# Optimization experiments

Hardware: AMD Instinct MI355X
Metric: run time of the kernel (lower is better)

## Reference

```python
import jax, jax.numpy as jnp
import numpy as np

N = 100000
E = 640000
IN_CH = 64
HID = 128
HEADS = [4, 4, 1]
BN_EPS = 1e-5
NEG_SLOPE = 0.2  # GATConv default leaky relu slope


def setup_inputs() -> dict:
    key = jax.random.key(0)
    ks = iter(jax.random.split(key, 48))
    nrm = lambda shape, s=0.1: jax.random.normal(next(ks), shape, jnp.float32) * s
    return dict(
        x=jax.random.normal(next(ks), (N, IN_CH), jnp.float32),
        edge_index=jax.random.randint(next(ks), (2, E), 0, N),
        edge_weight=jax.random.uniform(next(ks), (E,), jnp.float32),
        Wproj=nrm((IN_CH, HID)), bproj=jnp.zeros((HID,), jnp.float32),
        gat_W=nrm((3, HID, HID)), att_src=nrm((3, HID)), att_dst=nrm((3, HID)),
        att_edge=nrm((3, HID)), lin_edge_W=nrm((3, HID)),
        gat_bias=jnp.zeros((3, HID), jnp.float32),
        bn_gamma=jnp.ones((3, HID), jnp.float32), bn_beta=jnp.zeros((3, HID), jnp.float32),
        bn_mean=nrm((3, HID), 0.05),
        bn_var=jax.random.uniform(next(ks), (3, HID), jnp.float32, 0.5, 1.5),
        ew_W1=nrm((3, 32)), ew_b1=jnp.zeros((3, 32), jnp.float32),
        ew_W2=nrm((3, 32)), ew_b2=jnp.zeros((3,), jnp.float32),
        symptom_attention=jnp.ones((HID,), jnp.float32),
        clf_W1=nrm((HID, 64)), clf_b1=jnp.zeros((64,), jnp.float32),
        clf_bn_gamma=jnp.ones((64,), jnp.float32), clf_bn_beta=jnp.zeros((64,), jnp.float32),
        clf_bn_mean=nrm((64,), 0.05),
        clf_bn_var=jax.random.uniform(next(ks), (64,), jnp.float32, 0.5, 1.5),
        clf_W2=nrm((64, 32)), clf_b2=jnp.zeros((32,), jnp.float32),
        clf_W3=nrm((32, 2)), clf_b3=jnp.zeros((2,), jnp.float32),
    )


def _bn(x, g, b, m, v):
    # eval-mode BatchNorm with running stats
    return (x - m) * jax.lax.rsqrt(v + BN_EPS) * g + b


def reference(x, edge_index, edge_weight, Wproj, bproj, gat_W, att_src, att_dst,
              att_edge, lin_edge_W, gat_bias, bn_gamma, bn_beta, bn_mean, bn_var,
              ew_W1, ew_b1, ew_W2, ew_b2, symptom_attention, clf_W1, clf_b1,
              clf_bn_gamma, clf_bn_beta, clf_bn_mean, clf_bn_var, clf_W2, clf_b2,
              clf_W3, clf_b3):
    n = x.shape[0]
    loop = jnp.arange(n)
    src = jnp.concatenate([edge_index[0], loop])  # [E+N] self loops appended
    dst = jnp.concatenate([edge_index[1], loop])
    h = x @ Wproj + bproj  # input projection -> [N, HID]
    for i, H in enumerate(HEADS):
        C = HID // H
        # edge attention MLP: Linear(1,32)->ReLU->Linear(32,1)->Sigmoid on raw edge_weight
        eh = jax.nn.relu(edge_weight[:, None] * ew_W1[i][None, :] + ew_b1[i])
        ea = jax.nn.sigmoid(eh @ ew_W2[i] + ew_b2[i])  # [E]
        few = edge_weight * ea  # final edge weight [E]
        # self-loop edge attr fill_value='mean'
        e_attr = jnp.concatenate([few, jnp.broadcast_to(jnp.mean(few), (n,))])  # [E+N]
        # GATConv
        xl = (h @ gat_W[i]).reshape(n, H, C)
        a_src = jnp.sum(xl * att_src[i].reshape(H, C), axis=-1)  # [N,H]
        a_dst = jnp.sum(xl * att_dst[i].reshape(H, C), axis=-1)  # [N,H]
        e_lin = (e_attr[:, None] * lin_edge_W[i][None, :]).reshape(-1, H, C)
        a_edge = jnp.sum(e_lin * att_edge[i].reshape(H, C), axis=-1)  # [E+N,H]
        alpha = jax.nn.leaky_relu(a_src[src] + a_dst[dst] + a_edge, NEG_SLOPE)
        amax = jax.ops.segment_max(alpha, dst, num_segments=n)
        ex = jnp.exp(alpha - amax[dst])
        denom = jax.ops.segment_sum(ex, dst, num_segments=n)
        w = ex / (denom[dst] + 1e-16)  # segment softmax over incoming edges
        out = jax.ops.segment_sum(w[:, :, None] * xl[src], dst, num_segments=n)
        h = out.reshape(n, HID) + gat_bias[i]
        h = jax.nn.elu(_bn(h, bn_gamma[i], bn_beta[i], bn_mean[i], bn_var[i]))
        # dropout is identity in eval mode
    h = h * symptom_attention
    c = jax.nn.relu(h @ clf_W1 + clf_b1)
    c = _bn(c, clf_bn_gamma, clf_bn_beta, clf_bn_mean, clf_bn_var)
    c = jax.nn.relu(c @ clf_W2 + clf_b2)
    logits = c @ clf_W3 + clf_b3
    return logits
```

## Files before the change

### kernel.cpp

```cpp
#include <hip/hip_runtime.h>
#include <hip/hip_fp16.h>
#include <math.h>

#define NN 100000
#define EE 640000
#define ENL (EE + NN)
#define HIDD 128

constexpr float BN_EPS = 1e-5f;

template<int KDIM, int NC, int EPI, int H>
__global__ __launch_bounds__(256) void k_gemm(
    const float* __restrict__ A, const float* __restrict__ W,
    const float* __restrict__ bias, float* __restrict__ out, int nrows,
    const float* __restrict__ att_s, const float* __restrict__ att_d,
    float* __restrict__ a_src, float* __restrict__ a_dst,
    const float* __restrict__ bng, const float* __restrict__ bnb,
    const float* __restrict__ bnm, const float* __restrict__ bnv)
{
    constexpr int TXN = NC / 4;
    constexpr int TYN = 256 / TXN;
    constexpr int RPT = 64 / TYN;
    __shared__ float Al[64][36];
    __shared__ float Wl[32][NC];
    const int t = threadIdx.x;
    const int tx = t % TXN, ty = t / TXN;
    const long rowBase = (long)blockIdx.x * 64;
    float acc[RPT][4];
#pragma unroll
    for (int r = 0; r < RPT; ++r) { acc[r][0]=0.f; acc[r][1]=0.f; acc[r][2]=0.f; acc[r][3]=0.f; }

    for (int kk = 0; kk < KDIM; kk += 32) {
#pragma unroll
        for (int j = 0; j < 2; ++j) {
            int idx = t + j * 256;
            int r = idx >> 3;
            int k4 = (idx & 7) << 2;
            long gr = rowBase + r;
            float4 v = make_float4(0.f, 0.f, 0.f, 0.f);
            if (gr < nrows) v = *(const float4*)(A + gr * KDIM + kk + k4);
            *(float4*)&Al[r][k4] = v;
        }
        constexpr int WLOAD = (32 * NC / 4) / 256;
#pragma unroll
        for (int j = 0; j < WLOAD; ++j) {
            int idx = t + j * 256;
            int k = idx / TXN;
            int c4 = (idx % TXN) << 2;
            *(float4*)&Wl[k][c4] = *(const float4*)(W + (long)(kk + k) * NC + c4);
        }
        __syncthreads();
#pragma unroll
        for (int k = 0; k < 32; ++k) {
            float4 wv = *(float4*)&Wl[k][tx * 4];
#pragma unroll
            for (int r = 0; r < RPT; ++r) {
                float av = Al[ty * RPT + r][k];
                acc[r][0] = fmaf(av, wv.x, acc[r][0]);
                acc[r][1] = fmaf(av, wv.y, acc[r][1]);
                acc[r][2] = fmaf(av, wv.z, acc[r][2]);
                acc[r][3] = fmaf(av, wv.w, acc[r][3]);
            }
        }
        __syncthreads();
    }

    const int col0 = tx * 4;
    if constexpr (EPI == 0) {
        float4 b4 = *(const float4*)(bias + col0);
#pragma unroll
        for (int r = 0; r < RPT; ++r) {
            long row = rowBase + ty * RPT + r;
            if (row < nrows) {
                float4 o = make_float4(acc[r][0] + b4.x, acc[r][1] + b4.y,
                                       acc[r][2] + b4.z, acc[r][3] + b4.w);
                *(float4*)(out + row * NC + col0) = o;
            }
        }
    } else if constexpr (EPI == 1) {
        __half* outh = reinterpret_cast<__half*>(out);
        float as4[4], ad4[4];
#pragma unroll
        for (int c = 0; c < 4; ++c) { as4[c] = att_s[col0 + c]; ad4[c] = att_d[col0 + c]; }
        constexpr int G = TXN / H;
#pragma unroll
        for (int r = 0; r < RPT; ++r) {
            long row = rowBase + ty * RPT + r;
            if (row < nrows) {
                union { __half2 h2[2]; uint2 u; } pk;
                pk.h2[0] = __floats2half2_rn(acc[r][0], acc[r][1]);
                pk.h2[1] = __floats2half2_rn(acc[r][2], acc[r][3]);
                *(uint2*)(outh + row * NC + col0) = pk.u;
            }
            float ps = 0.f, pd = 0.f;
#pragma unroll
            for (int c = 0; c < 4; ++c) {
                ps = fmaf(acc[r][c], as4[c], ps);
                pd = fmaf(acc[r][c], ad4[c], pd);
            }
#pragma unroll
            for (int m_ = 1; m_ < G; m_ <<= 1) {
                ps += __shfl_xor(ps, m_, 64);
                pd += __shfl_xor(pd, m_, 64);
            }
            if ((tx & (G - 1)) == 0 && row < nrows) {
                int h = tx / G;
                a_src[row * H + h] = ps;
                a_dst[row * H + h] = pd;
            }
        }
    } else {
        float4 b4 = *(const float4*)(bias + col0);
        float4 g4 = *(const float4*)(bng + col0);
        float4 be4 = *(const float4*)(bnb + col0);
        float4 m4 = *(const float4*)(bnm + col0);
        float4 v4 = *(const float4*)(bnv + col0);
        float s0 = rsqrtf(v4.x + BN_EPS) * g4.x;
        float s1 = rsqrtf(v4.y + BN_EPS) * g4.y;
        float s2 = rsqrtf(v4.z + BN_EPS) * g4.z;
        float s3 = rsqrtf(v4.w + BN_EPS) * g4.w;
#pragma unroll
        for (int r = 0; r < RPT; ++r) {
            long row = rowBase + ty * RPT + r;
            if (row < nrows) {
                float o0 = fmaxf(acc[r][0] + b4.x, 0.f);
                float o1 = fmaxf(acc[r][1] + b4.y, 0.f);
                float o2 = fmaxf(acc[r][2] + b4.z, 0.f);
                float o3 = fmaxf(acc[r][3] + b4.w, 0.f);
                float4 o = make_float4((o0 - m4.x) * s0 + be4.x,
                                       (o1 - m4.y) * s1 + be4.y,
                                       (o2 - m4.z) * s2 + be4.z,
                                       (o3 - m4.w) * s3 + be4.w);
                *(float4*)(out + row * NC + col0) = o;
            }
        }
    }
}

__global__ void k_prep(const float* __restrict__ lew, const float* __restrict__ ae,
                       float* __restrict__ scal, int H)
{
    __shared__ float p[128];
    int t = threadIdx.x;
    p[t] = lew[t] * ae[t];
    __syncthreads();
    if (t == 0) scal[0] = 0.f;
    if (t < H) {
        int Cc = 128 / H;
        float s = 0.f;
        for (int c = 0; c < Cc; ++c) s += p[t * Cc + c];
        scal[4 + t] = s;
    }
}

__global__ __launch_bounds__(256) void k_edgemlp(
    const float* __restrict__ ew, const float* __restrict__ W1,
    const float* __restrict__ b1, const float* __restrict__ W2,
    const float* __restrict__ b2, float* __restrict__ few,
    float* __restrict__ sumfew)
{
    __shared__ float red[4];
    int e = blockIdx.x * 256 + threadIdx.x;
    float f = 0.f;
    if (e < EE) {
        float w = ew[e];
        float acc = b2[0];
#pragma unroll
        for (int j = 0; j < 32; ++j) {
            float t_ = fmaf(w, W1[j], b1[j]);
            t_ = fmaxf(t_, 0.f);
            acc = fmaf(t_, W2[j], acc);
        }
        f = w / (1.f + __expf(-acc));
        few[e] = f;
    }
    float s = f;
#pragma unroll
    for (int m_ = 1; m_ < 64; m_ <<= 1) s += __shfl_xor(s, m_, 64);
    int lane = threadIdx.x & 63, wid = threadIdx.x >> 6;
    if (lane == 0) red[wid] = s;
    __syncthreads();
    if (threadIdx.x == 0) atomicAdd(sumfew, red[0] + red[1] + red[2] + red[3]);
}

__global__ __launch_bounds__(256) void k_hist(const int* __restrict__ edst, int* __restrict__ cnt)
{
    int e = blockIdx.x * 256 + threadIdx.x;
    if (e < ENL) {
        int d = (e < EE) ? edst[e] : (e - EE);
        atomicAdd(&cnt[d], 1);
    }
}

__global__ __launch_bounds__(256) void k_scan1(const int* __restrict__ cnt,
                                               int* __restrict__ tmp, int* __restrict__ part)
{
    __shared__ int s1[256];
    int t = threadIdx.x;
    int i = blockIdx.x * 256 + t;
    int x = (i < NN) ? cnt[i] : 0;
    s1[t] = x;
    __syncthreads();
#pragma unroll
    for (int off = 1; off < 256; off <<= 1) {
        int v_ = (t >= off) ? s1[t - off] : 0;
        __syncthreads();
        s1[t] += v_;
        __syncthreads();
    }
    if (i < NN) tmp[i] = s1[t] - x;
    if (t == 255) part[blockIdx.x] = s1[255];
}

__global__ void k_scan2(int* __restrict__ part, int nb)
{
    __shared__ int s1[512];
    int t = threadIdx.x;
    int x = (t < nb) ? part[t] : 0;
    s1[t] = x;
    __syncthreads();
#pragma unroll
    for (int off = 1; off < 512; off <<= 1) {
        int v_ = (t >= off) ? s1[t - off] : 0;
        __syncthreads();
        s1[t] += v_;
        __syncthreads();
    }
    if (t < nb) part[t] = s1[t] - x;
}

__global__ __launch_bounds__(256) void k_scan3(int* __restrict__ rp, int* __restrict__ cur,
                                               const int* __restrict__ part)
{
    int i = blockIdx.x * 256 + threadIdx.x;
    if (i < NN) {
        int v_ = rp[i] + part[blockIdx.x];
        rp[i] = v_;
        cur[i] = v_;
    } else if (i == NN) {
        rp[NN] = ENL;
    }
}

__global__ __launch_bounds__(256) void k_scatter(const int* __restrict__ edst,
                                                 int* __restrict__ cur, int* __restrict__ eid)
{
    int e = blockIdx.x * 256 + threadIdx.x;
    if (e < ENL) {
        int d = (e < EE) ? edst[e] : (e - EE);
        int pos = atomicAdd(&cur[d], 1);
        eid[pos] = e;
    }
}

__global__ __launch_bounds__(256) void k_psrc(const int* __restrict__ eid,
                                              const int* __restrict__ esrc,
                                              int* __restrict__ ssrc)
{
    int p = blockIdx.x * 256 + threadIdx.x;
    if (p < ENL) {
        int e = eid[p];
        ssrc[p] = (e < EE) ? esrc[e] : (e - EE);
    }
}

__global__ __launch_bounds__(256) void k_pfew(const int* __restrict__ eid,
                                              const float* __restrict__ few,
                                              const float* __restrict__ scal,
                                              float* __restrict__ sfew)
{
    int p = blockIdx.x * 256 + threadIdx.x;
    if (p < ENL) {
        int e = eid[p];
        sfew[p] = (e < EE) ? few[e] : scal[0] * (1.0f / EE);
    }
}

template<int H>
__global__ __launch_bounds__(256) void k_agg(
    const __half* __restrict__ xl, const float* __restrict__ a_src,
    const float* __restrict__ a_dst, const float* __restrict__ sfew,
    const int* __restrict__ ssrc, const float* __restrict__ scal,
    const int* __restrict__ rp,
    const float* __restrict__ bias, const float* __restrict__ bng,
    const float* __restrict__ bnb, const float* __restrict__ bnm,
    const float* __restrict__ bnv, float* __restrict__ hout)
{
    const int lane = threadIdx.x & 63;
    const int n = (blockIdx.x << 2) + (threadIdx.x >> 6);
    if (n >= NN) return;
    float Kc[H], adn[H];
#pragma unroll
    for (int h = 0; h < H; ++h) { Kc[h] = scal[4 + h]; adn[h] = a_dst[n * H + h]; }
    const int p0 = rp[n];
    const int deg = rp[n + 1] - p0;

    float al[H], mx[H];
#pragma unroll
    for (int h = 0; h < H; ++h) { al[h] = -INFINITY; mx[h] = -INFINITY; }
    for (int base = 0; base < deg; base += 64) {
        int j = base + lane;
        float a_[H];
#pragma unroll
        for (int h = 0; h < H; ++h) a_[h] = -INFINITY;
        if (j < deg) {
            int s = ssrc[p0 + j];
            float ea = sfew[p0 + j];
            if constexpr (H == 4) {
                float4 as = *(const float4*)(a_src + s * 4);
                float x0 = as.x + adn[0] + ea * Kc[0];
                float x1 = as.y + adn[1] + ea * Kc[1];
                float x2 = as.z + adn[2] + ea * Kc[2];
                float x3 = as.w + adn[3] + ea * Kc[3];
                a_[0] = (x0 > 0.f) ? x0 : 0.2f * x0;
                a_[1] = (x1 > 0.f) ? x1 : 0.2f * x1;
                a_[2] = (x2 > 0.f) ? x2 : 0.2f * x2;
                a_[3] = (x3 > 0.f) ? x3 : 0.2f * x3;
            } else {
                float x0 = a_src[s] + adn[0] + ea * Kc[0];
                a_[0] = (x0 > 0.f) ? x0 : 0.2f * x0;
            }
        }
        if (base == 0) {
#pragma unroll
            for (int h = 0; h < H; ++h) al[h] = a_[h];
        }
#pragma unroll
        for (int h = 0; h < H; ++h) mx[h] = fmaxf(mx[h], a_[h]);
    }
#pragma unroll
    for (int h = 0; h < H; ++h) {
#pragma unroll
        for (int m_ = 1; m_ < 64; m_ <<= 1) mx[h] = fmaxf(mx[h], __shfl_xor(mx[h], m_, 64));
    }

    float dn[H];
#pragma unroll
    for (int h = 0; h < H; ++h) dn[h] = 0.f;
    if (deg <= 64) {
#pragma unroll
        for (int h = 0; h < H; ++h) dn[h] = (lane < deg) ? __expf(al[h] - mx[h]) : 0.f;
    } else {
        for (int base = 0; base < deg; base += 64) {
            int j = base + lane;
            if (j < deg) {
                int s = ssrc[p0 + j];
                float ea = sfew[p0 + j];
#pragma unroll
                for (int h = 0; h < H; ++h) {
                    float x_ = a_src[s * H + h] + adn[h] + ea * Kc[h];
                    x_ = (x_ > 0.f) ? x_ : 0.2f * x_;
                    dn[h] += __expf(x_ - mx[h]);
                }
            }
        }
    }
#pragma unroll
    for (int h = 0; h < H; ++h) {
#pragma unroll
        for (int m_ = 1; m_ < 64; m_ <<= 1) dn[h] += __shfl_xor(dn[h], m_, 64);
        dn[h] = 1.0f / (dn[h] + 1e-16f);
    }

    float acc0 = 0.f, acc1 = 0.f;
    for (int j = 0; j < deg; ++j) {
        int s = ssrc[p0 + j];
        float wsel;
        if (deg <= 64) {
            if constexpr (H == 4) {
                float a0 = __shfl(al[0], j, 64);
                float a1 = __shfl(al[1], j, 64);
                float a2 = __shfl(al[2], j, 64);
                float a3 = __shfl(al[3], j, 64);
                float w0 = __expf(a0 - mx[0]) * dn[0];
                float w1 = __expf(a1 - mx[1]) * dn[1];
                float w2 = __expf(a2 - mx[2]) * dn[2];
                float w3 = __expf(a3 - mx[3]) * dn[3];
                wsel = (lane < 16) ? w0 : ((lane < 32) ? w1 : ((lane < 48) ? w2 : w3));
            } else {
                float a0 = __shfl(al[0], j, 64);
                wsel = __expf(a0 - mx[0]) * dn[0];
            }
        } else {
            float ea = sfew[p0 + j];
            if constexpr (H == 4) {
                float4 as = *(const float4*)(a_src + s * 4);
                float x0 = as.x + adn[0] + ea * Kc[0]; x0 = (x0 > 0.f) ? x0 : 0.2f * x0;
                float x1 = as.y + adn[1] + ea * Kc[1]; x1 = (x1 > 0.f) ? x1 : 0.2f * x1;
                float x2 = as.z + adn[2] + ea * Kc[2]; x2 = (x2 > 0.f) ? x2 : 0.2f * x2;
                float x3 = as.w + adn[3] + ea * Kc[3]; x3 = (x3 > 0.f) ? x3 : 0.2f * x3;
                float w0 = __expf(x0 - mx[0]) * dn[0];
                float w1 = __expf(x1 - mx[1]) * dn[1];
                float w2 = __expf(x2 - mx[2]) * dn[2];
                float w3 = __expf(x3 - mx[3]) * dn[3];
                wsel = (lane < 16) ? w0 : ((lane < 32) ? w1 : ((lane < 48) ? w2 : w3));
            } else {
                float x0 = a_src[s] + adn[0] + ea * Kc[0]; x0 = (x0 > 0.f) ? x0 : 0.2f * x0;
                wsel = __expf(x0 - mx[0]) * dn[0];
            }
        }
        const __half2* xr = (const __half2*)(xl + (size_t)s * HIDD);
        float2 f = __half22float2(xr[lane]);
        acc0 = fmaf(wsel, f.x, acc0);
        acc1 = fmaf(wsel, f.y, acc1);
    }

    {
        int c0 = 2 * lane;
        float2 bi = *(const float2*)(bias + c0);
        float2 g  = *(const float2*)(bng + c0);
        float2 bb = *(const float2*)(bnb + c0);
        float2 mm = *(const float2*)(bnm + c0);
        float2 vv = *(const float2*)(bnv + c0);
        float o0 = acc0 + bi.x;
        o0 = (o0 - mm.x) * rsqrtf(vv.x + BN_EPS) * g.x + bb.x;
        o0 = (o0 > 0.f) ? o0 : (__expf(o0) - 1.f);
        float o1 = acc1 + bi.y;
        o1 = (o1 - mm.y) * rsqrtf(vv.y + BN_EPS) * g.y + bb.y;
        o1 = (o1 > 0.f) ? o1 : (__expf(o1) - 1.f);
        *(float2*)(hout + (size_t)n * HIDD + c0) = make_float2(o0, o1);
    }
}

__global__ void k_scaleW1(const float* __restrict__ W1, const float* __restrict__ sym,
                          float* __restrict__ W1s)
{
    int i = blockIdx.x * 256 + threadIdx.x;
    if (i < 128 * 64) W1s[i] = W1[i] * sym[i >> 6];
}

__global__ __launch_bounds__(256) void k_clf2(const float* __restrict__ c1,
                                              const float* __restrict__ W2,
                                              const float* __restrict__ b2,
                                              float* __restrict__ c2)
{
    __shared__ float Wl[64][32];
    int t = threadIdx.x;
#pragma unroll
    for (int j = 0; j < 2; ++j) {
        int idx = t + j * 256;
        ((float4*)Wl)[idx] = ((const float4*)W2)[idx];
    }
    __syncthreads();
    int n = blockIdx.x * 256 + t;
    if (n >= NN) return;
    float acc[32];
#pragma unroll
    for (int j = 0; j < 32; ++j) acc[j] = b2[j];
    const float* row = c1 + (long)n * 64;
#pragma unroll
    for (int k0 = 0; k0 < 64; k0 += 4) {
        float4 hv = *(const float4*)(row + k0);
#pragma unroll
        for (int kk = 0; kk < 4; ++kk) {
            float h_ = (&hv.x)[kk];
#pragma unroll
            for (int j4 = 0; j4 < 8; ++j4) {
                float4 w4 = *(float4*)&Wl[k0 + kk][j4 * 4];
                acc[j4 * 4 + 0] = fmaf(h_, w4.x, acc[j4 * 4 + 0]);
                acc[j4 * 4 + 1] = fmaf(h_, w4.y, acc[j4 * 4 + 1]);
                acc[j4 * 4 + 2] = fmaf(h_, w4.z, acc[j4 * 4 + 2]);
                acc[j4 * 4 + 3] = fmaf(h_, w4.w, acc[j4 * 4 + 3]);
            }
        }
    }
    float* o = c2 + (long)n * 32;
#pragma unroll
    for (int j4 = 0; j4 < 8; ++j4) {
        float4 v = make_float4(fmaxf(acc[j4 * 4 + 0], 0.f), fmaxf(acc[j4 * 4 + 1], 0.f),
                               fmaxf(acc[j4 * 4 + 2], 0.f), fmaxf(acc[j4 * 4 + 3], 0.f));
        *(float4*)(o + j4 * 4) = v;
    }
}

__global__ __launch_bounds__(256) void k_clf3(const float* __restrict__ c2,
                                              const float* __restrict__ W3,
                                              const float* __restrict__ b3,
                                              float* __restrict__ out)
{
    int n = blockIdx.x * 256 + threadIdx.x;
    if (n >= NN) return;
    const float* row = c2 + (long)n * 32;
    float l0 = b3[0], l1 = b3[1];
#pragma unroll
    for (int k = 0; k < 32; ++k) {
        float cv = row[k];
        l0 = fmaf(cv, W3[k * 2 + 0], l0);
        l1 = fmaf(cv, W3[k * 2 + 1], l1);
    }
    *(float2*)(out + (long)n * 2) = make_float2(l0, l1);
}

extern "C" void kernel_launch(void* const* d_in, const int* in_sizes, int n_in,
                              void* d_out, int out_size, void* d_ws, size_t ws_size,
                              hipStream_t stream)
{
    const float* x          = (const float*)d_in[0];
    const int*   edge_index = (const int*)d_in[1];
    const float* edge_w     = (const float*)d_in[2];
    const float* Wproj      = (const float*)d_in[3];
    const float* bproj      = (const float*)d_in[4];
    const float* gat_W      = (const float*)d_in[5];
    const float* att_src    = (const float*)d_in[6];
    const float* att_dst    = (const float*)d_in[7];
    const float* att_edge   = (const float*)d_in[8];
    const float* lin_edge_W = (const float*)d_in[9];
    const float* gat_bias   = (const float*)d_in[10];
    const float* bn_g       = (const float*)d_in[11];
    const float* bn_b       = (const float*)d_in[12];
    const float* bn_m       = (const float*)d_in[13];
    const float* bn_v       = (const float*)d_in[14];
    const float* ew_W1      = (const float*)d_in[15];
    const float* ew_b1      = (const float*)d_in[16];
    const float* ew_W2      = (const float*)d_in[17];
    const float* ew_b2      = (const float*)d_in[18];
    const float* sym        = (const float*)d_in[19];
    const float* clf_W1     = (const float*)d_in[20];
    const float* clf_b1     = (const float*)d_in[21];
    const float* clf_bng    = (const float*)d_in[22];
    const float* clf_bnb    = (const float*)d_in[23];
    const float* clf_bnm    = (const float*)d_in[24];
    const float* clf_bnv    = (const float*)d_in[25];
    const float* clf_W2     = (const float*)d_in[26];
    const float* clf_b2     = (const float*)d_in[27];
    const float* clf_W3     = (const float*)d_in[28];
    const float* clf_b3     = (const float*)d_in[29];
    float* outp = (float*)d_out;

    float* ws   = (float*)d_ws;
    float* hbuf = ws;
    float* xlf  = hbuf + 12800000;
    __half* xl  = (__half*)xlf;
    float* c1   = xlf;
    int*   ssrc = (int*)(xlf + 6400000);
    float* sfew = xlf + 7200000;
    float* c2   = xlf + 6400000;
    float* asrc = xlf + 12800000;
    float* adst = asrc + 400000;
    float* fewp = adst + 400000;
    float* scal = fewp + 640000;
    float* W1s  = scal + 16;
    int* rp   = (int*)(W1s + 8192);
    int* cur  = rp + 100004;
    int* eid  = cur + 100000;
    int* part = eid + 740000;

    const int* esrc = edge_index;
    const int* edst = edge_index + EE;

    hipMemsetAsync(cur, 0, NN * sizeof(int), stream);

    k_gemm<64, 128, 0, 1><<<1563, 256, 0, stream>>>(
        x, Wproj, bproj, hbuf, NN,
        nullptr, nullptr, nullptr, nullptr, nullptr, nullptr, nullptr, nullptr);

    k_hist<<<2891, 256, 0, stream>>>(edst, cur);
    k_scan1<<<391, 256, 0, stream>>>(cur, rp, part);
    k_scan2<<<1, 512, 0, stream>>>(part, 391);
    k_scan3<<<391, 256, 0, stream>>>(rp, cur, part);
    k_scatter<<<2891, 256, 0, stream>>>(edst, cur, eid);
    k_psrc<<<2891, 256, 0, stream>>>(eid, esrc, ssrc);

    for (int i = 0; i < 3; ++i) {
        int H = (i == 2) ? 1 : 4;
        k_prep<<<1, 128, 0, stream>>>(lin_edge_W + i * 128, att_edge + i * 128, scal, H);
        k_edgemlp<<<2500, 256, 0, stream>>>(edge_w, ew_W1 + i * 32, ew_b1 + i * 32,
                                            ew_W2 + i * 32, ew_b2 + i, fewp, scal);
        k_pfew<<<2891, 256, 0, stream>>>(eid, fewp, scal, sfew);
        if (H == 4) {
            k_gemm<128, 128, 1, 4><<<1563, 256, 0, stream>>>(
                hbuf, gat_W + i * 128 * 128, nullptr, xlf, NN,
                att_src + i * 128, att_dst + i * 128, asrc, adst,
                nullptr, nullptr, nullptr, nullptr);
            k_agg<4><<<25000, 256, 0, stream>>>(
                xl, asrc, adst, sfew, ssrc, scal, rp,
                gat_bias + i * 128, bn_g + i * 128, bn_b + i * 128,
                bn_m + i * 128, bn_v + i * 128, hbuf);
        } else {
            k_gemm<128, 128, 1, 1><<<1563, 256, 0, stream>>>(
                hbuf, gat_W + i * 128 * 128, nullptr, xlf, NN,
                att_src + i * 128, att_dst + i * 128, asrc, adst,
                nullptr, nullptr, nullptr, nullptr);
            k_agg<1><<<25000, 256, 0, stream>>>(
                xl, asrc, adst, sfew, ssrc, scal, rp,
                gat_bias + i * 128, bn_g + i * 128, bn_b + i * 128,
                bn_m + i * 128, bn_v + i * 128, hbuf);
        }
    }

    k_scaleW1<<<32, 256, 0, stream>>>(clf_W1, sym, W1s);
    k_gemm<128, 64, 2, 1><<<1563, 256, 0, stream>>>(
        hbuf, W1s, clf_b1, c1, NN,
        nullptr, nullptr, nullptr, nullptr, clf_bng, clf_bnb, clf_bnm, clf_bnv);
    k_clf2<<<391, 256, 0, stream>>>(c1, clf_W2, clf_b2, c2);
    k_clf3<<<391, 256, 0, stream>>>(c2, clf_W3, clf_b3, outp);
}
```

Before: 913.8 us.

## Precompute softmax weights into shared memory and unroll gather loop in aggregation

For nodes with at most 64 incoming edges, the aggregation kernel now computes normalized attention weights once per lane and stores them in shared memory. This replaces the per-edge shuffles and exps in the gather loop with LDS reads. The gather loop is unrolled by four so several xl row loads can be in flight at once. The early return for out-of-range nodes is removed to allow a block-wide __syncthreads, which adds a barrier and relies on NN being a multiple of 4 for safe indexing.

```diff
diff --git a/kernel.cpp b/kernel.cpp
--- a/kernel.cpp
+++ b/kernel.cpp
@@ -286,61 +286,90 @@
     const float* __restrict__ bnb, const float* __restrict__ bnm,
     const float* __restrict__ bnv, float* __restrict__ hout)
 {
+    __shared__ float lw[4][H][66];
     const int lane = threadIdx.x & 63;
-    const int n = (blockIdx.x << 2) + (threadIdx.x >> 6);
-    if (n >= NN) return;
+    const int wid  = threadIdx.x >> 6;
+    const int n = (blockIdx.x << 2) + wid;
     float Kc[H], adn[H];
 #pragma unroll
     for (int h = 0; h < H; ++h) { Kc[h] = scal[4 + h]; adn[h] = a_dst[n * H + h]; }
     const int p0 = rp[n];
     const int deg = rp[n + 1] - p0;
-
-    float al[H], mx[H];
-#pragma unroll
-    for (int h = 0; h < H; ++h) { al[h] = -INFINITY; mx[h] = -INFINITY; }
-    for (int base = 0; base < deg; base += 64) {
-        int j = base + lane;
-        float a_[H];
-#pragma unroll
-        for (int h = 0; h < H; ++h) a_[h] = -INFINITY;
-        if (j < deg) {
-            int s = ssrc[p0 + j];
-            float ea = sfew[p0 + j];
+    const bool fast = (deg <= 64);
+
+    float acc0 = 0.f, acc1 = 0.f;
+
+    if (fast) {
+        const bool act = lane < deg;
+        float al[H];
+        if (act) {
+            int s = ssrc[p0 + lane];
+            float ea = sfew[p0 + lane];
             if constexpr (H == 4) {
                 float4 as = *(const float4*)(a_src + s * 4);
                 float x0 = as.x + adn[0] + ea * Kc[0];
                 float x1 = as.y + adn[1] + ea * Kc[1];
                 float x2 = as.z + adn[2] + ea * Kc[2];
                 float x3 = as.w + adn[3] + ea * Kc[3];
-                a_[0] = (x0 > 0.f) ? x0 : 0.2f * x0;
-                a_[1] = (x1 > 0.f) ? x1 : 0.2f * x1;
-                a_[2] = (x2 > 0.f) ? x2 : 0.2f * x2;
-                a_[3] = (x3 > 0.f) ? x3 : 0.2f * x3;
+                al[0] = (x0 > 0.f) ? x0 : 0.2f * x0;
+                al[1] = (x1 > 0.f) ? x1 : 0.2f * x1;
+                al[2] = (x2 > 0.f) ? x2 : 0.2f * x2;
+                al[3] = (x3 > 0.f) ? x3 : 0.2f * x3;
             } else {
                 float x0 = a_src[s] + adn[0] + ea * Kc[0];
-                a_[0] = (x0 > 0.f) ? x0 : 0.2f * x0;
-            }
-        }
-        if (base == 0) {
-#pragma unroll
-            for (int h = 0; h < H; ++h) al[h] = a_[h];
-        }
-#pragma unroll
-        for (int h = 0; h < H; ++h) mx[h] = fmaxf(mx[h], a_[h]);
-    }
-#pragma unroll
-    for (int h = 0; h < H; ++h) {
-#pragma unroll
-        for (int m_ = 1; m_ < 64; m_ <<= 1) mx[h] = fmaxf(mx[h], __shfl_xor(mx[h], m_, 64));
-    }
-
-    float dn[H];
-#pragma unroll
-    for (int h = 0; h < H; ++h) dn[h] = 0.f;
-    if (deg <= 64) {
-#pragma unroll
-        for (int h = 0; h < H; ++h) dn[h] = (lane < deg) ? __expf(al[h] - mx[h]) : 0.f;
+                al[0] = (x0 > 0.f) ? x0 : 0.2f * x0;
+            }
+        } else {
+#pragma unroll
+            for (int h = 0; h < H; ++h) al[h] = -INFINITY;
+        }
+        float mx[H], ex[H], dn[H];
+#pragma unroll
+        for (int h = 0; h < H; ++h) {
+            mx[h] = al[h];
+#pragma unroll
+            for (int m_ = 1; m_ < 64; m_ <<= 1) mx[h] = fmaxf(mx[h], __shfl_xor(mx[h], m_, 64));
+        }
+#pragma unroll
+        for (int h = 0; h < H; ++h) {
+            ex[h] = act ? __expf(al[h] - mx[h]) : 0.f;
+            dn[h] = ex[h];
+#pragma unroll
+            for (int m_ = 1; m_ < 64; m_ <<= 1) dn[h] += __shfl_xor(dn[h], m_, 64);
+            lw[wid][h][lane] = ex[h] * (1.0f / (dn[h] + 1e-16f));
+        }
+    }
+    __syncthreads();
+
+    if (fast) {
+        const int myh = (H == 4) ? (lane >> 4) : 0;
+        const float* wrow = &lw[wid][myh][0];
+        int j = 0;
+        for (; j + 4 <= deg; j += 4) {
+            int s0 = ssrc[p0 + j + 0];
+            int s1 = ssrc[p0 + j + 1];
+            int s2 = ssrc[p0 + j + 2];
+            int s3 = ssrc[p0 + j + 3];
+            float w0 = wrow[j + 0], w1 = wrow[j + 1], w2 = wrow[j + 2], w3 = wrow[j + 3];
+            float2 f0 = __half22float2(((const __half2*)(xl + (size_t)s0 * HIDD))[lane]);
+            float2 f1 = __half22float2(((const __half2*)(xl + (size_t)s1 * HIDD))[lane]);
+            float2 f2 = __half22float2(((const __half2*)(xl + (size_t)s2 * HIDD))[lane]);
+            float2 f3 = __half22float2(((const __half2*)(xl + (size_t)s3 * HIDD))[lane]);
+            acc0 = fmaf(w0, f0.x, acc0); acc1 = fmaf(w0, f0.y, acc1);
+            acc0 = fmaf(w1, f1.x, acc0); acc1 = fmaf(w1, f1.y, acc1);
+            acc0 = fmaf(w2, f2.x, acc0); acc1 = fmaf(w2, f2.y, acc1);
+            acc0 = fmaf(w3, f3.x, acc0); acc1 = fmaf(w3, f3.y, acc1);
+        }
+        for (; j < deg; ++j) {
+            int s0 = ssrc[p0 + j];
+            float w0 = wrow[j];
+            float2 f0 = __half22float2(((const __half2*)(xl + (size_t)s0 * HIDD))[lane]);
+            acc0 = fmaf(w0, f0.x, acc0); acc1 = fmaf(w0, f0.y, acc1);
+        }
     } else {
+        float mx[H], dn[H];
+#pragma unroll
+        for (int h = 0; h < H; ++h) mx[h] = -INFINITY;
         for (int base = 0; base < deg; base += 64) {
             int j = base + lane;
             if (j < deg) {
@@ -350,39 +379,39 @@
                 for (int h = 0; h < H; ++h) {
                     float x_ = a_src[s * H + h] + adn[h] + ea * Kc[h];
                     x_ = (x_ > 0.f) ? x_ : 0.2f * x_;
+                    mx[h] = fmaxf(mx[h], x_);
+                }
+            }
+        }
+#pragma unroll
+        for (int h = 0; h < H; ++h) {
+#pragma unroll
+            for (int m_ = 1; m_ < 64; m_ <<= 1) mx[h] = fmaxf(mx[h], __shfl_xor(mx[h], m_, 64));
+            dn[h] = 0.f;
+        }
+        for (int base = 0; base < deg; base += 64) {
+            int j = base + lane;
+            if (j < deg) {
+                int s = ssrc[p0 + j];
+                float ea = sfew[p0 + j];
+#pragma unroll
+                for (int h = 0; h < H; ++h) {
+                    float x_ = a_src[s * H + h] + adn[h] + ea * Kc[h];
+                    x_ = (x_ > 0.f) ? x_ : 0.2f * x_;
                     dn[h] += __expf(x_ - mx[h]);
                 }
             }
         }
-    }
-#pragma unroll
-    for (int h = 0; h < H; ++h) {
-#pragma unroll
-        for (int m_ = 1; m_ < 64; m_ <<= 1) dn[h] += __shfl_xor(dn[h], m_, 64);
-        dn[h] = 1.0f / (dn[h] + 1e-16f);
-    }
-
-    float acc0 = 0.f, acc1 = 0.f;
-    for (int j = 0; j < deg; ++j) {
-        int s = ssrc[p0 + j];
-        float wsel;
-        if (deg <= 64) {
-            if constexpr (H == 4) {
-                float a0 = __shfl(al[0], j, 64);
-                float a1 = __shfl(al[1], j, 64);
-                float a2 = __shfl(al[2], j, 64);
-                float a3 = __shfl(al[3], j, 64);
-                float w0 = __expf(a0 - mx[0]) * dn[0];
-                float w1 = __expf(a1 - mx[1]) * dn[1];
-                float w2 = __expf(a2 - mx[2]) * dn[2];
-                float w3 = __expf(a3 - mx[3]) * dn[3];
-                wsel = (lane < 16) ? w0 : ((lane < 32) ? w1 : ((lane < 48) ? w2 : w3));
-            } else {
-                float a0 = __shfl(al[0], j, 64);
-                wsel = __expf(a0 - mx[0]) * dn[0];
-            }
-        } else {
+#pragma unroll
+        for (int h = 0; h < H; ++h) {
+#pragma unroll
+            for (int m_ = 1; m_ < 64; m_ <<= 1) dn[h] += __shfl_xor(dn[h], m_, 64);
+            dn[h] = 1.0f / (dn[h] + 1e-16f);
+        }
+        for (int j = 0; j < deg; ++j) {
+            int s = ssrc[p0 + j];
             float ea = sfew[p0 + j];
+            float wsel;
             if constexpr (H == 4) {
                 float4 as = *(const float4*)(a_src + s * 4);
                 float x0 = as.x + adn[0] + ea * Kc[0]; x0 = (x0 > 0.f) ? x0 : 0.2f * x0;
@@ -398,11 +427,10 @@
                 float x0 = a_src[s] + adn[0] + ea * Kc[0]; x0 = (x0 > 0.f) ? x0 : 0.2f * x0;
                 wsel = __expf(x0 - mx[0]) * dn[0];
             }
-        }
-        const __half2* xr = (const __half2*)(xl + (size_t)s * HIDD);
-        float2 f = __half22float2(xr[lane]);
-        acc0 = fmaf(wsel, f.x, acc0);
-        acc1 = fmaf(wsel, f.y, acc1);
+            float2 f = __half22float2(((const __half2*)(xl + (size_t)s * HIDD))[lane]);
+            acc0 = fmaf(wsel, f.x, acc0);
+            acc1 = fmaf(wsel, f.y, acc1);
+        }
     }
 
     {
```

Measured after the change: 784.2 us. 14.2% less time.
